# Performance work log

Hardware: AMD Instinct MI355X
Metric: run time of the kernel (lower is better)

The kernel has to match this reference:

```python
import jax, jax.numpy as jnp
import numpy as np

MIMO_RANK = 4  # module constant; q/k are identical across rank and mimo_v=mimo_out=ones,
               # q_bias=k_bias=0, so the rank sum equals MIMO_RANK * single-rank output.


def _rotary(t, ang):
    # split-half rotary: t [..., d], ang [..., d//2]
    d2 = t.shape[-1] // 2
    t1, t2 = t[..., :d2], t[..., d2:]
    c, s = jnp.cos(ang), jnp.sin(ang)
    return jnp.concatenate([t1 * c - t2 * s, t1 * s + t2 * c], axis=-1)


def setup_inputs() -> dict:
    key = jax.random.key(0)
    ks = jax.random.split(key, 6)
    b, l, h, dv, g, dqk = 2, 4096, 32, 64, 1, 128
    x = jax.random.normal(ks[0], (b, l, h, dv), jnp.float32)
    # positive step sizes (discretization dt)
    dt = jax.random.uniform(ks[1], (b, l, h), jnp.float32) * 0.05 + 1e-3
    # negative decay rates so exp(A*dt) < 1
    A = -(jax.random.uniform(ks[2], (h,), jnp.float32) + 0.5)
    B_gate = jax.random.normal(ks[3], (b, l, g, dqk), jnp.float32)
    C_gate = jax.random.normal(ks[4], (b, l, g, dqk), jnp.float32)
    D = jax.random.normal(ks[5], (h,), jnp.float32)
    return {"x": x, "dt": dt, "A": A, "B_gate": B_gate, "C_gate": C_gate,
            "D": D, "chunk_size": 64}


def reference(x, dt, A, B_gate, C_gate, D, chunk_size):
    # Mamba3 MIMO chunked selective scan (SSD) with rotary QK decay.
    # Recurrence per (b, h):  H_t = exp(A_h*dt_t) * H_{t-1} + rot(k_t) (dt_t x_t)^T
    #                         y_t = rot(q_t)^T H_t * MIMO_RANK + D_h * x_t
    # where q=C_gate, k=B_gate (shared across heads, ngroups=1) and the rotary
    # angle is theta_t = cumsum(dt) (TILELANG_ROTARY_DIV=2 -> dqk//2 angles).
    b, l, h, dv = x.shape
    dqk = C_gate.shape[-1]
    c = chunk_size
    n = l // c

    ang = jnp.cumsum(dt, axis=1)[..., None]                     # [b,l,h,1]
    ang = jnp.broadcast_to(ang, (b, l, h, dqk // 2))
    q = jnp.broadcast_to(C_gate[:, :, 0, :][:, :, None, :], (b, l, h, dqk))
    k = jnp.broadcast_to(B_gate[:, :, 0, :][:, :, None, :], (b, l, h, dqk))
    rotq = _rotary(q, ang)                                      # [b,l,h,dqk]
    rotk = _rotary(k, ang)
    adt = A[None, None, :] * dt                                 # [b,l,h] log-decay

    chunk = lambda t: t.reshape(b, n, c, *t.shape[2:])
    rq, rk = chunk(rotq), chunk(rotk)                           # [b,n,c,h,dqk]
    u = chunk(dt[..., None] * x)                                # [b,n,c,h,dv]
    a = chunk(adt)                                              # [b,n,c,h]
    cum = jnp.cumsum(a, axis=2)                                 # within-chunk cum log-decay

    # ---- intra-chunk (quadratic within chunk) ----
    seg = cum[:, :, :, None, :] - cum[:, :, None, :, :]         # [b,n,t,s,h]
    mask = jnp.tril(jnp.ones((c, c), bool))
    L = jnp.where(mask[None, None, :, :, None], jnp.exp(seg), 0.0)
    S = jnp.einsum('bnthd,bnshd->bntsh', rq, rk)                # [b,n,t,s,h]
    y_intra = jnp.einsum('bntsh,bnshe->bnthe', S * L, u)        # [b,n,c,h,dv]

    # ---- inter-chunk state recurrence ----
    decay_to_end = jnp.exp(cum[:, :, -1:, :] - cum)             # [b,n,c,h]
    dH = jnp.einsum('bnshd,bnsh,bnshe->bnhde', rk, decay_to_end, u)  # [b,n,h,dqk,dv]
    cdecay = jnp.exp(cum[:, :, -1, :])                          # [b,n,h] full-chunk decay

    def step(H, inp):
        dc, dh = inp
        Hprev = H
        return dc[:, :, None, None] * H + dh, Hprev

    H0 = jnp.zeros((b, h, dqk, dv), x.dtype)
    _, Hprev = jax.lax.scan(step, H0,
                            (jnp.moveaxis(cdecay, 1, 0), jnp.moveaxis(dH, 1, 0)))
    Hprev = jnp.moveaxis(Hprev, 0, 1)                           # [b,n,h,dqk,dv]

    y_inter = jnp.einsum('bnthd,bnth,bnhde->bnthe', rq, jnp.exp(cum), Hprev)

    y = MIMO_RANK * (y_intra + y_inter).reshape(b, l, h, dv)
    return y + D[None, None, :, None] * x
```

## Files before the change

### kernel.cpp

```cpp
#include <hip/hip_runtime.h>
#include <hip/hip_bf16.h>

#define BB 2
#define LL 4096
#define HH 32
#define DV 64
#define DQK 128
#define CC 64
#define NN 64
#define MIMO_RANK 4.0f

typedef __attribute__((ext_vector_type(8))) short short8;
typedef __attribute__((ext_vector_type(4))) float f32x4;

__device__ __forceinline__ ushort f2bf(float f) {
    uint u = __float_as_uint(f);
    u += 0x7FFF + ((u >> 16) & 1);
    return (ushort)(u >> 16);
}
__device__ __forceinline__ float bfbits2f(uint lo16) {
    return __uint_as_float(lo16 << 16);
}
__device__ __forceinline__ uint pkbf2(float lo, float hi) {
    return (uint)f2bf(lo) | ((uint)f2bf(hi) << 16);
}
union U8 { uint u[4]; short8 s; };

__device__ __forceinline__ int rk_off(int s, int d) {
    return s * 128 + (((((d >> 3) & 15) ^ (s & 7)) << 3)) + (d & 7);
}
__device__ __forceinline__ int uwT_off(int e, int s) {
    return e * 64 + ((((s >> 3) ^ (e & 7)) & 7) << 3) + (s & 7);
}
__device__ __forceinline__ int fSL(int t) {
    return (((t & 3) << 1) ^ ((t >> 2) & 7)) & 7;
}
__device__ __forceinline__ int SL_off(int t, int s) {
    return t * 64 + ((((s >> 3) ^ fSL(t)) & 7) << 3) + (s & 7);
}

__device__ __forceinline__ void make_rot_frags(const float* __restrict__ G,
                                               size_t gb, float cv, float sv,
                                               int kgrp, short8* fr) {
    #pragma unroll
    for (int kk = 0; kk < 4; ++kk) {
        int d0 = kk * 32 + kgrp;
        int dl = d0 & 63;
        bool low = d0 < 64;
        float4 a1 = *(const float4*)(G + gb + dl);
        float4 b1 = *(const float4*)(G + gb + dl + 4);
        float4 a2 = *(const float4*)(G + gb + dl + 64);
        float4 b2 = *(const float4*)(G + gb + dl + 68);
        float v0, v1, v2, v3, v4, v5, v6, v7;
        if (low) {
            v0 = a1.x * cv - a2.x * sv; v1 = a1.y * cv - a2.y * sv;
            v2 = a1.z * cv - a2.z * sv; v3 = a1.w * cv - a2.w * sv;
            v4 = b1.x * cv - b2.x * sv; v5 = b1.y * cv - b2.y * sv;
            v6 = b1.z * cv - b2.z * sv; v7 = b1.w * cv - b2.w * sv;
        } else {
            v0 = a1.x * sv + a2.x * cv; v1 = a1.y * sv + a2.y * cv;
            v2 = a1.z * sv + a2.z * cv; v3 = a1.w * sv + a2.w * cv;
            v4 = b1.x * sv + b2.x * cv; v5 = b1.y * sv + b2.y * cv;
            v6 = b1.z * sv + b2.z * cv; v7 = b1.w * sv + b2.w * cv;
        }
        U8 r;
        r.u[0] = pkbf2(v0, v1); r.u[1] = pkbf2(v2, v3);
        r.u[2] = pkbf2(v4, v5); r.u[3] = pkbf2(v6, v7);
        fr[kk] = r.s;
    }
}

__global__ __launch_bounds__(256) void k_scan_dt(const float* __restrict__ dt,
                                                 const float* __restrict__ A,
                                                 float4* __restrict__ tbl,
                                                 float* __restrict__ cdecay) {
    int bh = blockIdx.x;
    int b = bh / HH, h = bh % HH;
    int tid = threadIdx.x;
    const int PT = LL / 256;
    float v[PT];
    float s = 0.f;
    int tbase = tid * PT;
    for (int i = 0; i < PT; ++i) {
        v[i] = dt[(((size_t)b * LL + tbase + i) * HH) + h];
        s += v[i];
    }
    int lane = tid & 63, wv = tid >> 6;
    float ps = s;
    for (int off = 1; off < 64; off <<= 1) {
        float o = __shfl_up(ps, off, 64);
        if (lane >= off) ps += o;
    }
    __shared__ float wsum[4];
    if (lane == 63) wsum[wv] = ps;
    __syncthreads();
    float wadd = 0.f;
    for (int w = 0; w < wv; ++w) wadd += wsum[w];
    float run0 = wadd + ps - s;
    float run_end = run0 + s;
    float aend  = __shfl(run_end, lane | 3, 64);
    float aprev = __shfl(run0, lane & ~3, 64);
    float Ah = A[h];
    if ((tid & 3) == 0) {
        int n = tid >> 2;
        cdecay[(b * NN + n) * HH + h] = __expf(Ah * (aend - aprev));
    }
    float4* tb = tbl + ((size_t)(b * HH + h) * LL) + tbase;
    float run = run0;
    for (int i = 0; i < PT; ++i) {
        run += v[i];
        float sv, cv;
        __sincosf(run, &sv, &cv);
        float dw = __expf(Ah * (aend - run));
        float et = __expf(Ah * (run - aend));
        tb[i] = make_float4(cv, sv, v[i] * dw, et);
    }
}

__global__ __launch_bounds__(256, 3) void k_intra(
    const float* __restrict__ x, const float* __restrict__ Bg,
    const float* __restrict__ Cg, const float4* __restrict__ tbl,
    const float* __restrict__ Dd,
    float* __restrict__ out, ushort* __restrict__ dH) {
    int n = blockIdx.x, h = blockIdx.y, b = blockIdx.z;
    int tid = threadIdx.x;
    int t0 = n * CC;

    __shared__ ushort rkS[CC * DQK];
    __shared__ ushort uwT[DV * CC];
    __shared__ float4 tblLds[CC];
    __shared__ float  xraw[CC * DV];

    int wv = tid >> 6, lane = tid & 63;
    int lrow = lane & 15;
    int g = lane >> 4;
    int kgrp = g * 8;
    int orow = g * 4;

    const float* BgRow = Bg + ((size_t)b * LL + t0) * DQK;

    {
        const float4* tbsrc = tbl + ((size_t)(b * HH + h) * LL) + t0 + lane;
        __builtin_amdgcn_global_load_lds((const void*)tbsrc, (void*)tblLds,
                                         16, 0, 0);
    }
    #pragma unroll
    for (int i = 0; i < 4; ++i) {
        int row = 16 * wv + 4 * i + (lane >> 4);
        const float* xsrc = x + ((((size_t)b * LL + t0 + row) * HH) + h) * DV
                            + 4 * (lane & 15);
        __builtin_amdgcn_global_load_lds((const void*)xsrc,
                                         (void*)(xraw + (16 * wv + 4 * i) * DV),
                                         16, 0, 0);
    }
    float4 bg0[2], bg1[2], bg2[2], bg3[2];
    #pragma unroll
    for (int it = 0; it < 2; ++it) {
        int s = (tid >> 3) + 32 * it, oct = tid & 7;
        const float* p = BgRow + s * DQK + 8 * oct;
        bg0[it] = *(const float4*)(p);
        bg1[it] = *(const float4*)(p + 4);
        bg2[it] = *(const float4*)(p + 64);
        bg3[it] = *(const float4*)(p + 68);
    }

    asm volatile("s_waitcnt vmcnt(0)" ::: "memory");
    __builtin_amdgcn_sched_barrier(0);

    int t_own = 16 * wv + lrow;
    float4 tq = tblLds[t_own];
    short8 aq[4];
    make_rot_frags(Cg, ((size_t)b * LL + t0 + t_own) * DQK, tq.x, tq.y, kgrp, aq);

    #pragma unroll
    for (int it = 0; it < 2; ++it) {
        int s = (tid >> 3) + 32 * it, oct = tid & 7;
        float4 tv = tblLds[s];
        float cv = tv.x, sv = tv.y;
        U8 lo, hi;
        lo.u[0] = pkbf2(bg0[it].x * cv - bg2[it].x * sv, bg0[it].y * cv - bg2[it].y * sv);
        lo.u[1] = pkbf2(bg0[it].z * cv - bg2[it].z * sv, bg0[it].w * cv - bg2[it].w * sv);
        lo.u[2] = pkbf2(bg1[it].x * cv - bg3[it].x * sv, bg1[it].y * cv - bg3[it].y * sv);
        lo.u[3] = pkbf2(bg1[it].z * cv - bg3[it].z * sv, bg1[it].w * cv - bg3[it].w * sv);
        hi.u[0] = pkbf2(bg0[it].x * sv + bg2[it].x * cv, bg0[it].y * sv + bg2[it].y * cv);
        hi.u[1] = pkbf2(bg0[it].z * sv + bg2[it].z * cv, bg0[it].w * sv + bg2[it].w * cv);
        hi.u[2] = pkbf2(bg1[it].x * sv + bg3[it].x * cv, bg1[it].y * sv + bg3[it].y * cv);
        hi.u[3] = pkbf2(bg1[it].z * sv + bg3[it].z * cv, bg1[it].w * sv + bg3[it].w * cv);
        *(short8*)&rkS[rk_off(s, 8 * oct)] = lo.s;
        *(short8*)&rkS[rk_off(s, 8 * oct + 64)] = hi.s;
    }

    #pragma unroll
    for (int it = 0; it < 2; ++it) {
        int s0 = 16 * wv + 8 * it;
        int e = lane;
        U8 pk;
        #pragma unroll
        for (int jp = 0; jp < 4; ++jp) {
            int sa = s0 + 2 * jp, sb = sa + 1;
            float xa = xraw[sa * DV + e] * tblLds[sa].z;
            float xb = xraw[sb * DV + e] * tblLds[sb].z;
            pk.u[jp] = pkbf2(xa, xb);
        }
        *(short8*)&uwT[uwT_off(e, s0)] = pk.s;
    }

    __syncthreads();

    f32x4 accS[4] = {{0.f,0.f,0.f,0.f},{0.f,0.f,0.f,0.f},
                     {0.f,0.f,0.f,0.f},{0.f,0.f,0.f,0.f}};
    #pragma unroll
    for (int kk = 0; kk < 4; ++kk) {
        #pragma unroll
        for (int nt = 0; nt < 4; ++nt) {
            int s = 16 * nt + lrow;
            const short8 bfr = *(const short8*)&rkS[rk_off(s, 32 * kk + kgrp)];
            accS[nt] = __builtin_amdgcn_mfma_f32_16x16x32_bf16(
                aq[kk], bfr, accS[nt], 0, 0, 0);
        }
    }

    short8 aH[2][2];
    #pragma unroll
    for (int kk = 0; kk < 2; ++kk) {
        #pragma unroll
        for (int mt = 0; mt < 2; ++mt) {
            int d = 32 * wv + 16 * mt + lrow;
            uint vv[8];
            #pragma unroll
            for (int j = 0; j < 8; ++j)
                vv[j] = rkS[rk_off(32 * kk + kgrp + j, d)];
            U8 pk;
            pk.u[0] = vv[0] | (vv[1] << 16);
            pk.u[1] = vv[2] | (vv[3] << 16);
            pk.u[2] = vv[4] | (vv[5] << 16);
            pk.u[3] = vv[6] | (vv[7] << 16);
            aH[kk][mt] = pk.s;
        }
    }

    __syncthreads();

    ushort* SLs = rkS;
    #pragma unroll
    for (int rr = 0; rr < 4; ++rr) {
        int t = 16 * wv + orow + rr;
        float etv = tblLds[t].w;
        #pragma unroll
        for (int nt = 0; nt < 4; ++nt) {
            int s = 16 * nt + lrow;
            float v = (t >= s) ? accS[nt][rr] * etv : 0.f;
            SLs[SL_off(t, s)] = f2bf(v);
        }
    }

    __syncthreads();

    {
        f32x4 accY[4] = {{0.f,0.f,0.f,0.f},{0.f,0.f,0.f,0.f},
                         {0.f,0.f,0.f,0.f},{0.f,0.f,0.f,0.f}};
        #pragma unroll
        for (int kk = 0; kk < 2; ++kk) {
            const short8 a = *(const short8*)&SLs[SL_off(16 * wv + lrow, 32 * kk + kgrp)];
            #pragma unroll
            for (int nt = 0; nt < 4; ++nt) {
                const short8 bfr = *(const short8*)&uwT[uwT_off(16 * nt + lrow, 32 * kk + kgrp)];
                accY[nt] = __builtin_amdgcn_mfma_f32_16x16x32_bf16(
                    a, bfr, accY[nt], 0, 0, 0);
            }
        }
        float Dh = Dd[h];
        #pragma unroll
        for (int nt = 0; nt < 4; ++nt) {
            int e = 16 * nt + lrow;
            #pragma unroll
            for (int rr = 0; rr < 4; ++rr) {
                int t = 16 * wv + orow + rr;
                size_t oidx = ((((size_t)b * LL + t0 + t) * HH) + h) * DV + e;
                out[oidx] = MIMO_RANK * accY[nt][rr] + Dh * xraw[t * DV + e];
            }
        }
    }

    {
        f32x4 accH[2][4] = {{{0.f,0.f,0.f,0.f},{0.f,0.f,0.f,0.f},
                             {0.f,0.f,0.f,0.f},{0.f,0.f,0.f,0.f}},
                            {{0.f,0.f,0.f,0.f},{0.f,0.f,0.f,0.f},
                             {0.f,0.f,0.f,0.f},{0.f,0.f,0.f,0.f}}};
        #pragma unroll
        for (int kk = 0; kk < 2; ++kk) {
            #pragma unroll
            for (int mt = 0; mt < 2; ++mt) {
                #pragma unroll
                for (int nt = 0; nt < 4; ++nt) {
                    const short8 bfr = *(const short8*)&uwT[uwT_off(16 * nt + lrow, 32 * kk + kgrp)];
                    accH[mt][nt] = __builtin_amdgcn_mfma_f32_16x16x32_bf16(
                        aH[kk][mt], bfr, accH[mt][nt], 0, 0, 0);
                }
            }
        }
        ushort* dHp = dH + (((size_t)(b * NN + n) * HH) + h) * (DQK * DV);
        #pragma unroll
        for (int q = 0; q < 4; ++q) {
            int mt = q >> 1, np = q & 1;
            U8 st;
            st.u[0] = pkbf2(accH[mt][2 * np][0], accH[mt][2 * np][1]);
            st.u[1] = pkbf2(accH[mt][2 * np][2], accH[mt][2 * np][3]);
            st.u[2] = pkbf2(accH[mt][2 * np + 1][0], accH[mt][2 * np + 1][1]);
            st.u[3] = pkbf2(accH[mt][2 * np + 1][2], accH[mt][2 * np + 1][3]);
            *(short8*)(dHp + ((size_t)(wv * 4 + q) * 64 + lane) * 8) = st.s;
        }
    }
}

__global__ __launch_bounds__(256) void k_scan_chunks(
    uint* __restrict__ dH, const float* __restrict__ cdecay) {
    uint f = blockIdx.x * 256 + threadIdx.x;
    int b = (int)(f >> 17);
    uint r = f & 0x1FFFF;
    int h = (int)((r >> 12) & 31);
    uint base = ((uint)b << 23) | r;
    const float* cd = cdecay + (size_t)b * NN * HH + h;
    float h0 = 0.f, h1 = 0.f;
    for (int n = 0; n < NN; ++n) {
        uint a = base + ((uint)n << 17);
        uint v = dH[a];
        float v0 = bfbits2f(v & 0xFFFF), v1 = bfbits2f(v >> 16);
        dH[a] = pkbf2(h0, h1);
        float c = cd[n * HH];
        h0 = c * h0 + v0;
        h1 = c * h1 + v1;
    }
}

__global__ __launch_bounds__(256, 6) void k_inter(
    const float* __restrict__ Cg, const float4* __restrict__ tbl,
    const float* __restrict__ cdecay, const ushort* __restrict__ Hprev,
    float* __restrict__ out) {
    int n = blockIdx.x, h = blockIdx.y, b = blockIdx.z;
    int tid = threadIdx.x;
    int t0 = n * CC;

    __shared__ __align__(16) uint Hp[16 * 260];

    const float4* tb = tbl + ((size_t)(b * HH + h) * LL) + t0;
    float cdec = cdecay[(b * NN + n) * HH + h];

    const uint* Hsrc = (const uint*)(Hprev + (((size_t)(b * NN + n) * HH) + h) * (DQK * DV));
    #pragma unroll
    for (int it = 0; it < 4; ++it) {
        int p = tid + 256 * it;
        uint4 v = *(const uint4*)(Hsrc + (size_t)p * 4);
        int row = p >> 6, c = p & 63;
        uint4* Hrow = (uint4*)&Hp[row * 260];
        Hrow[c] = v;
    }

    int wv = tid >> 6, lane = tid & 63;
    int lrow = lane & 15;
    int g2 = lane >> 4;
    int kgrp = g2 * 8;
    int orow = g2 * 4;

    int t_own = 16 * wv + lrow;
    float4 tq = tb[t_own];
    short8 aq[4];
    make_rot_frags(Cg, ((size_t)b * LL + t0 + t_own) * DQK, tq.x, tq.y, kgrp, aq);
    __syncthreads();

    f32x4 accI[4] = {{0.f,0.f,0.f,0.f},{0.f,0.f,0.f,0.f},
                     {0.f,0.f,0.f,0.f},{0.f,0.f,0.f,0.f}};
    int mt = g2 >> 1;
    int gp0 = 2 * (g2 & 1);
    #pragma unroll
    for (int kk = 0; kk < 4; ++kk) {
        #pragma unroll
        for (int nt = 0; nt < 4; ++nt) {
            int q = mt * 2 + (nt >> 1);
            int row = kk * 4 + q;
            int sb = (nt & 1) * 2;
            const uint2 u0 = *(const uint2*)&Hp[row * 260 + (16 * gp0 + lrow) * 4 + sb];
            const uint2 u1 = *(const uint2*)&Hp[row * 260 + (16 * (gp0 + 1) + lrow) * 4 + sb];
            U8 fr;
            fr.u[0] = u0.x; fr.u[1] = u0.y; fr.u[2] = u1.x; fr.u[3] = u1.y;
            accI[nt] = __builtin_amdgcn_mfma_f32_16x16x32_bf16(
                aq[kk], fr.s, accI[nt], 0, 0, 0);
        }
    }

    #pragma unroll
    for (int rr = 0; rr < 4; ++rr) {
        int t = 16 * wv + orow + rr;
        float g4 = MIMO_RANK * tb[t].w * cdec;
        #pragma unroll
        for (int nt = 0; nt < 4; ++nt) {
            int e = 16 * nt + lrow;
            size_t oidx = ((((size_t)b * LL + t0 + t) * HH) + h) * DV + e;
            out[oidx] += g4 * accI[nt][rr];
        }
    }
}

extern "C" void kernel_launch(void* const* d_in, const int* in_sizes, int n_in,
                              void* d_out, int out_size, void* d_ws,
                              size_t ws_size, hipStream_t stream) {
    (void)in_sizes; (void)n_in; (void)out_size; (void)ws_size;
    const float* x  = (const float*)d_in[0];
    const float* dt = (const float*)d_in[1];
    const float* A  = (const float*)d_in[2];
    const float* Bg = (const float*)d_in[3];
    const float* Cg = (const float*)d_in[4];
    const float* Dd = (const float*)d_in[5];
    float* out = (float*)d_out;
    float* ws  = (float*)d_ws;

    float4* tbl    = (float4*)ws;
    float*  cdecay = ws + (size_t)BB * HH * LL * 4;
    ushort* dH     = (ushort*)(cdecay + BB * NN * HH);

    k_scan_dt<<<BB * HH, 256, 0, stream>>>(dt, A, tbl, cdecay);
    k_intra<<<dim3(NN, HH, BB), 256, 0, stream>>>(x, Bg, Cg, tbl, Dd, out, dH);
    k_scan_chunks<<<(BB * HH * DQK * DV / 2) / 256, 256, 0, stream>>>(
        (uint*)dH, cdecay);
    k_inter<<<dim3(NN, HH, BB), 256, 0, stream>>>(Cg, tbl, cdecay, dH, out);
}
```

Before: 113.7 us.

## Store intra-chunk output as bf16 temp and widen chunk scan to 4 elems

The intra-chunk kernel now writes its partial output (including the D*x skip term) as bf16 to a workspace buffer instead of fp32 to the output. The inter kernel reads that buffer and writes the final output once, which removes the fp32 read-modify-write of the output. The chunk-state scan now handles four bf16 values per thread with 8-byte accesses, halving its thread count, and bf16 rounding now uses the library conversion. Rounding the intra part to bf16 adds precision loss to the output.

```diff
diff --git a/kernel.cpp b/kernel.cpp
--- a/kernel.cpp
+++ b/kernel.cpp
@@ -14,9 +14,8 @@
 typedef __attribute__((ext_vector_type(4))) float f32x4;
 
 __device__ __forceinline__ ushort f2bf(float f) {
-    uint u = __float_as_uint(f);
-    u += 0x7FFF + ((u >> 16) & 1);
-    return (ushort)(u >> 16);
+    __hip_bfloat16 h = __float2bfloat16(f);
+    return *reinterpret_cast<ushort*>(&h);
 }
 __device__ __forceinline__ float bfbits2f(uint lo16) {
     return __uint_as_float(lo16 << 16);
@@ -121,7 +120,7 @@
     const float* __restrict__ x, const float* __restrict__ Bg,
     const float* __restrict__ Cg, const float4* __restrict__ tbl,
     const float* __restrict__ Dd,
-    float* __restrict__ out, ushort* __restrict__ dH) {
+    ushort* __restrict__ ytmp, ushort* __restrict__ dH) {
     int n = blockIdx.x, h = blockIdx.y, b = blockIdx.z;
     int tid = threadIdx.x;
     int t0 = n * CC;
@@ -277,7 +276,7 @@
             for (int rr = 0; rr < 4; ++rr) {
                 int t = 16 * wv + orow + rr;
                 size_t oidx = ((((size_t)b * LL + t0 + t) * HH) + h) * DV + e;
-                out[oidx] = MIMO_RANK * accY[nt][rr] + Dh * xraw[t * DV + e];
+                ytmp[oidx] = f2bf(MIMO_RANK * accY[nt][rr] + Dh * xraw[t * DV + e]);
             }
         }
     }
@@ -314,29 +313,33 @@
 }
 
 __global__ __launch_bounds__(256) void k_scan_chunks(
-    uint* __restrict__ dH, const float* __restrict__ cdecay) {
+    uint2* __restrict__ dH, const float* __restrict__ cdecay) {
     uint f = blockIdx.x * 256 + threadIdx.x;
-    int b = (int)(f >> 17);
-    uint r = f & 0x1FFFF;
-    int h = (int)((r >> 12) & 31);
-    uint base = ((uint)b << 23) | r;
+    int b = (int)(f >> 16);
+    uint pos = f & 0xFFFF;
+    int h = (int)((pos >> 11) & 31);
+    uint base = ((uint)b << 22) + pos;
     const float* cd = cdecay + (size_t)b * NN * HH + h;
-    float h0 = 0.f, h1 = 0.f;
+    float h0 = 0.f, h1 = 0.f, h2 = 0.f, h3 = 0.f;
     for (int n = 0; n < NN; ++n) {
-        uint a = base + ((uint)n << 17);
-        uint v = dH[a];
-        float v0 = bfbits2f(v & 0xFFFF), v1 = bfbits2f(v >> 16);
-        dH[a] = pkbf2(h0, h1);
+        uint a = base + ((uint)n << 16);
+        uint2 v = dH[a];
+        float v0 = bfbits2f(v.x & 0xFFFF), v1 = bfbits2f(v.x >> 16);
+        float v2 = bfbits2f(v.y & 0xFFFF), v3 = bfbits2f(v.y >> 16);
+        uint2 st;
+        st.x = pkbf2(h0, h1);
+        st.y = pkbf2(h2, h3);
+        dH[a] = st;
         float c = cd[n * HH];
-        h0 = c * h0 + v0;
-        h1 = c * h1 + v1;
+        h0 = c * h0 + v0; h1 = c * h1 + v1;
+        h2 = c * h2 + v2; h3 = c * h3 + v3;
     }
 }
 
 __global__ __launch_bounds__(256, 6) void k_inter(
     const float* __restrict__ Cg, const float4* __restrict__ tbl,
     const float* __restrict__ cdecay, const ushort* __restrict__ Hprev,
-    float* __restrict__ out) {
+    const ushort* __restrict__ ytmp, float* __restrict__ out) {
     int n = blockIdx.x, h = blockIdx.y, b = blockIdx.z;
     int tid = threadIdx.x;
     int t0 = n * CC;
@@ -396,7 +399,7 @@
         for (int nt = 0; nt < 4; ++nt) {
             int e = 16 * nt + lrow;
             size_t oidx = ((((size_t)b * LL + t0 + t) * HH) + h) * DV + e;
-            out[oidx] += g4 * accI[nt][rr];
+            out[oidx] = bfbits2f(ytmp[oidx]) + g4 * accI[nt][rr];
         }
     }
 }
@@ -417,10 +420,11 @@
     float4* tbl    = (float4*)ws;
     float*  cdecay = ws + (size_t)BB * HH * LL * 4;
     ushort* dH     = (ushort*)(cdecay + BB * NN * HH);
+    ushort* ytmp   = dH + (size_t)BB * NN * HH * DQK * DV;
 
     k_scan_dt<<<BB * HH, 256, 0, stream>>>(dt, A, tbl, cdecay);
-    k_intra<<<dim3(NN, HH, BB), 256, 0, stream>>>(x, Bg, Cg, tbl, Dd, out, dH);
-    k_scan_chunks<<<(BB * HH * DQK * DV / 2) / 256, 256, 0, stream>>>(
-        (uint*)dH, cdecay);
-    k_inter<<<dim3(NN, HH, BB), 256, 0, stream>>>(Cg, tbl, cdecay, dH, out);
-}
+    k_intra<<<dim3(NN, HH, BB), 256, 0, stream>>>(x, Bg, Cg, tbl, Dd, ytmp, dH);
+    k_scan_chunks<<<(BB * NN * HH * DQK * DV / 4 / NN) / 256, 256, 0, stream>>>(
+        (uint2*)dH, cdecay);
+    k_inter<<<dim3(NN, HH, BB), 256, 0, stream>>>(Cg, tbl, cdecay, dH, ytmp, out);
+}
```

Result: slower. 116.2 us (+2.2%).

## Stage intra-chunk output as bf16 scratch instead of fp32 read-modify-write

Applied to the files above, without the earlier changes.

The intra-chunk kernel no longer writes fp32 output. It writes its partial result, including the D*x term, as bf16 in a fragment-ordered scratch buffer with coalesced 16-byte stores. The inter kernel then reads that scratch and writes the final output once, replacing the fp32 read-modify-write on the output and cutting global traffic. In exchange it adds a bf16 rounding of the intra part, a little more accuracy loss, and lowers k_inter's launch-bounds occupancy hint from 6 to 4 blocks.

```diff
diff --git a/kernel.cpp b/kernel.cpp
--- a/kernel.cpp
+++ b/kernel.cpp
@@ -14,9 +14,8 @@
 typedef __attribute__((ext_vector_type(4))) float f32x4;
 
 __device__ __forceinline__ ushort f2bf(float f) {
-    uint u = __float_as_uint(f);
-    u += 0x7FFF + ((u >> 16) & 1);
-    return (ushort)(u >> 16);
+    __hip_bfloat16 h = __float2bfloat16(f);
+    return *reinterpret_cast<ushort*>(&h);
 }
 __device__ __forceinline__ float bfbits2f(uint lo16) {
     return __uint_as_float(lo16 << 16);
@@ -121,7 +120,7 @@
     const float* __restrict__ x, const float* __restrict__ Bg,
     const float* __restrict__ Cg, const float4* __restrict__ tbl,
     const float* __restrict__ Dd,
-    float* __restrict__ out, ushort* __restrict__ dH) {
+    ushort* __restrict__ ytmp, ushort* __restrict__ dH) {
     int n = blockIdx.x, h = blockIdx.y, b = blockIdx.z;
     int tid = threadIdx.x;
     int t0 = n * CC;
@@ -270,15 +269,25 @@
             }
         }
         float Dh = Dd[h];
+        float fin[4][4];
         #pragma unroll
         for (int nt = 0; nt < 4; ++nt) {
             int e = 16 * nt + lrow;
             #pragma unroll
             for (int rr = 0; rr < 4; ++rr) {
                 int t = 16 * wv + orow + rr;
-                size_t oidx = ((((size_t)b * LL + t0 + t) * HH) + h) * DV + e;
-                out[oidx] = MIMO_RANK * accY[nt][rr] + Dh * xraw[t * DV + e];
+                fin[nt][rr] = MIMO_RANK * accY[nt][rr] + Dh * xraw[t * DV + e];
             }
+        }
+        ushort* ytp = ytmp + (((size_t)(b * NN + n) * HH) + h) * (CC * DV);
+        #pragma unroll
+        for (int q = 0; q < 2; ++q) {
+            U8 st;
+            st.u[0] = pkbf2(fin[2 * q][0], fin[2 * q][1]);
+            st.u[1] = pkbf2(fin[2 * q][2], fin[2 * q][3]);
+            st.u[2] = pkbf2(fin[2 * q + 1][0], fin[2 * q + 1][1]);
+            st.u[3] = pkbf2(fin[2 * q + 1][2], fin[2 * q + 1][3]);
+            *(short8*)(ytp + ((size_t)(wv * 2 + q) * 64 + lane) * 8) = st.s;
         }
     }
 
@@ -333,10 +342,10 @@
     }
 }
 
-__global__ __launch_bounds__(256, 6) void k_inter(
+__global__ __launch_bounds__(256, 4) void k_inter(
     const float* __restrict__ Cg, const float4* __restrict__ tbl,
     const float* __restrict__ cdecay, const ushort* __restrict__ Hprev,
-    float* __restrict__ out) {
+    const ushort* __restrict__ ytmp, float* __restrict__ out) {
     int n = blockIdx.x, h = blockIdx.y, b = blockIdx.z;
     int tid = threadIdx.x;
     int t0 = n * CC;
@@ -345,6 +354,17 @@
 
     const float4* tb = tbl + ((size_t)(b * HH + h) * LL) + t0;
     float cdec = cdecay[(b * NN + n) * HH + h];
+
+    int wv = tid >> 6, lane = tid & 63;
+    int lrow = lane & 15;
+    int g2 = lane >> 4;
+    int kgrp = g2 * 8;
+    int orow = g2 * 4;
+
+    const ushort* ytp = ytmp + (((size_t)(b * NN + n) * HH) + h) * (CC * DV);
+    U8 y0, y1;
+    y0.s = *(const short8*)(ytp + ((size_t)(wv * 2 + 0) * 64 + lane) * 8);
+    y1.s = *(const short8*)(ytp + ((size_t)(wv * 2 + 1) * 64 + lane) * 8);
 
     const uint* Hsrc = (const uint*)(Hprev + (((size_t)(b * NN + n) * HH) + h) * (DQK * DV));
     #pragma unroll
@@ -355,12 +375,6 @@
         uint4* Hrow = (uint4*)&Hp[row * 260];
         Hrow[c] = v;
     }
-
-    int wv = tid >> 6, lane = tid & 63;
-    int lrow = lane & 15;
-    int g2 = lane >> 4;
-    int kgrp = g2 * 8;
-    int orow = g2 * 4;
 
     int t_own = 16 * wv + lrow;
     float4 tq = tb[t_own];
@@ -395,8 +409,11 @@
         #pragma unroll
         for (int nt = 0; nt < 4; ++nt) {
             int e = 16 * nt + lrow;
+            uint bits = (nt < 2) ? y0.u[(nt & 1) * 2 + (rr >> 1)]
+                                 : y1.u[(nt & 1) * 2 + (rr >> 1)];
+            float yv = bfbits2f((rr & 1) ? (bits >> 16) : (bits & 0xFFFF));
             size_t oidx = ((((size_t)b * LL + t0 + t) * HH) + h) * DV + e;
-            out[oidx] += g4 * accI[nt][rr];
+            out[oidx] = yv + g4 * accI[nt][rr];
         }
     }
 }
@@ -417,10 +434,11 @@
     float4* tbl    = (float4*)ws;
     float*  cdecay = ws + (size_t)BB * HH * LL * 4;
     ushort* dH     = (ushort*)(cdecay + BB * NN * HH);
+    ushort* ytmp   = dH + (size_t)BB * NN * HH * DQK * DV;
 
     k_scan_dt<<<BB * HH, 256, 0, stream>>>(dt, A, tbl, cdecay);
-    k_intra<<<dim3(NN, HH, BB), 256, 0, stream>>>(x, Bg, Cg, tbl, Dd, out, dH);
+    k_intra<<<dim3(NN, HH, BB), 256, 0, stream>>>(x, Bg, Cg, tbl, Dd, ytmp, dH);
     k_scan_chunks<<<(BB * HH * DQK * DV / 2) / 256, 256, 0, stream>>>(
         (uint*)dH, cdecay);
-    k_inter<<<dim3(NN, HH, BB), 256, 0, stream>>>(Cg, tbl, cdecay, dH, out);
-}
+    k_inter<<<dim3(NN, HH, BB), 256, 0, stream>>>(Cg, tbl, cdecay, dH, ytmp, out);
+}
```

Result: faster. 104.3 us (-8.3%).
